# Kernel optimization log

Hardware: AMD Instinct MI355X
Metric: run time of the kernel (lower is better)

The kernel has to match this reference:

```python
import jax, jax.numpy as jnp
import numpy as np

POS_W, NEG_W = 2.0, 40.0
MARGIN, THRESH = 0.1, 0.5


def setup_inputs() -> dict:
    key = jax.random.key(0)
    k1, k2 = jax.random.split(key)
    B, D, C = 4096, 128, 100
    batch = jax.random.normal(k1, (B, D), dtype=jnp.float32)
    # metric-learning embeddings are L2-normalized -> sim in [-1, 1]
    batch = batch / jnp.linalg.norm(batch, axis=1, keepdims=True)
    labels = jax.random.randint(k2, (B,), 0, C)
    return {"batch": batch, "labels": labels}


def reference(batch, labels):
    B = batch.shape[0]
    sim = batch @ batch.T  # [B, B]
    eq = labels[:, None] == labels[None, :]
    not_self = ~jnp.eye(B, dtype=bool)
    pos_mask = eq & not_self   # positives, excluding anchor itself
    neg_mask = ~eq             # negatives

    # per-row hardest thresholds (masked min/max)
    min_pos = jnp.min(jnp.where(pos_mask, sim, jnp.inf), axis=1)   # [B]
    max_neg = jnp.max(jnp.where(neg_mask, sim, -jnp.inf), axis=1)  # [B]

    neg_keep = neg_mask & (sim + MARGIN > min_pos[:, None])
    pos_keep = pos_mask & (sim - MARGIN < max_neg[:, None])

    # masked exponentials: exp(-inf) = 0 keeps it overflow-safe
    pos_sum = jnp.sum(jnp.exp(jnp.where(pos_keep, -POS_W * (sim - THRESH), -jnp.inf)), axis=1)
    neg_sum = jnp.sum(jnp.exp(jnp.where(neg_keep, NEG_W * (sim - THRESH), -jnp.inf)), axis=1)

    row_loss = jnp.log1p(pos_sum) / POS_W + jnp.log1p(neg_sum) / NEG_W  # [B]

    # original skips rows where either kept-set is empty
    valid = jnp.any(pos_keep, axis=1) & jnp.any(neg_keep, axis=1)
    n_valid = jnp.maximum(jnp.sum(valid), 1)
    return jnp.sum(jnp.where(valid, row_loss, 0.0)) / n_valid
```

## Files before the change

kernel.cpp:

```cpp
#include <hip/hip_runtime.h>
#include <math.h>

#define Bsz 4096
#define Dk 128
#define RPB 32
#define CS 16
#define CPB (Bsz / CS)
#define THREADS 256
#define WAVES 4
#define CPW (CPB / WAVES)
#define CT (CPW / 16)
#define RT (RPB / 16)

typedef __attribute__((ext_vector_type(8))) short short8;
typedef __attribute__((ext_vector_type(4))) float f32x4;

__device__ __forceinline__ unsigned short f2bf(float f) {
  unsigned u = __float_as_uint(f);
  u = (u + 0x7fffu + ((u >> 16) & 1u)) >> 16;
  return (unsigned short)u;
}

__global__ __launch_bounds__(256)
void convert_kernel(const float* __restrict__ X, short* __restrict__ Xt) {
  int i = blockIdx.x * 256 + threadIdx.x;
  int col = i >> 4, kb = i & 15;
  const float4* q = (const float4*)(X + col * Dk + kb * 8);
  float4 v0 = q[0], v1 = q[1];
  short8 r;
  r[0] = (short)f2bf(v0.x); r[1] = (short)f2bf(v0.y);
  r[2] = (short)f2bf(v0.z); r[3] = (short)f2bf(v0.w);
  r[4] = (short)f2bf(v1.x); r[5] = (short)f2bf(v1.y);
  r[6] = (short)f2bf(v1.z); r[7] = (short)f2bf(v1.w);
  *(short8*)(Xt + (size_t)(kb * Bsz + col) * 8) = r;
}

__device__ __forceinline__ short8 ldfrag(const short* __restrict__ Xt, int col, int ks, int lg) {
  return *(const short8*)(Xt + (size_t)(((ks << 2) + lg) * Bsz + col) * 8);
}

template<int PHASE>
__global__ __launch_bounds__(THREADS, 4)
void sweep(const short* __restrict__ Xt, const int* __restrict__ labels,
           const float* __restrict__ min_part, const float* __restrict__ max_part,
           float* __restrict__ out0, float* __restrict__ out1,
           float* __restrict__ vld) {
  const int tid = threadIdx.x;
  const int w  = tid >> 6;
  const int l  = tid & 63;
  const int lg = l >> 4;
  const int lr = l & 15;
  const int by = blockIdx.x / CS;
  const int bx = blockIdx.x % CS;
  const int r0 = by * RPB;
  const int c0 = bx * CPB + w * CPW;

  __shared__ float red[2][WAVES][RPB];
  __shared__ float thp_s[RPB], thn_s[RPB];

  if (PHASE == 1) {
    if (tid < RPB) {
      int r = r0 + tid;
      float mnr = INFINITY, mxr = -INFINITY;
#pragma unroll
      for (int b = 0; b < CS; ++b) {
        mnr = fminf(mnr, min_part[b * Bsz + r]);
        mxr = fmaxf(mxr, max_part[b * Bsz + r]);
      }
      thp_s[tid] = mxr + 0.1f;
      thn_s[tid] = mnr - 0.1f;
      if (bx == 0) vld[r] = (mnr - 0.1f < mxr) ? 1.0f : 0.0f;
    }
  }

  short8 afrag[RT][4];
  for (int rt = 0; rt < RT; ++rt)
    for (int ks = 0; ks < 4; ++ks)
      afrag[rt][ks] = ldfrag(Xt, r0 + rt * 16 + lr, ks, lg);

  int labr[RT * 4];
  for (int rt = 0; rt < RT; ++rt)
    for (int rg = 0; rg < 4; ++rg)
      labr[rt * 4 + rg] = labels[r0 + rt * 16 + lg * 4 + rg];

  float tp[RT * 4], tn[RT * 4];
  if (PHASE == 1) {
    __syncthreads();
    for (int rt = 0; rt < RT; ++rt)
      for (int rg = 0; rg < 4; ++rg) {
        int rl = rt * 16 + lg * 4 + rg;
        tp[rt * 4 + rg] = thp_s[rl];
        tn[rt * 4 + rg] = thn_s[rl];
      }
  }

  float a0[RT * 4], a1[RT * 4];
  for (int i = 0; i < RT * 4; ++i) {
    a0[i] = (PHASE == 0) ? INFINITY  : 0.f;
    a1[i] = (PHASE == 0) ? -INFINITY : 0.f;
  }

#pragma unroll
  for (int ct = 0; ct < CT; ++ct) {
    const int ctc  = c0 + ct * 16;
    const int colv = ctc + lr;
    short8 bfrag[4];
    for (int ks = 0; ks < 4; ++ks) bfrag[ks] = ldfrag(Xt, colv, ks, lg);
    const int labc = labels[colv];

    for (int rt = 0; rt < RT; ++rt) {
      f32x4 acc = {0.f, 0.f, 0.f, 0.f};
      for (int ks = 0; ks < 4; ++ks)
        acc = __builtin_amdgcn_mfma_f32_16x16x32_bf16(afrag[rt][ks], bfrag[ks], acc, 0, 0, 0);
      const bool diag = (ctc == r0 + rt * 16);
      for (int rg = 0; rg < 4; ++rg) {
        int   i    = rt * 4 + rg;
        float s    = acc[rg];
        bool  eq   = (labc == labr[i]);
        bool  self = diag && (lr == lg * 4 + rg);
        if (PHASE == 0) {
          if (eq && !self) a0[i] = fminf(a0[i], s);
          if (!eq)         a1[i] = fmaxf(a1[i], s);
        } else {
          bool  kp   = eq && !self && (s < tp[i]);
          bool  kn   = (!eq) && (s > tn[i]);
          float argp = fmaf(s, -2.885390082f, 1.442695041f);
          float argn = fmaf(s, 57.70780163f, -28.85390082f);
          float e = exp2f(kp ? argp : argn);
          a0[i] += kp ? e : 0.f;
          a1[i] += kn ? e : 0.f;
        }
      }
    }
  }

  for (int i = 0; i < RT * 4; ++i) {
    for (int m = 1; m < 16; m <<= 1) {
      float o0 = __shfl_xor(a0[i], m, 64);
      float o1 = __shfl_xor(a1[i], m, 64);
      if (PHASE == 0) { a0[i] = fminf(a0[i], o0); a1[i] = fmaxf(a1[i], o1); }
      else            { a0[i] += o0;              a1[i] += o1; }
    }
  }
  if (lr == 0)
    for (int i = 0; i < RT * 4; ++i) {
      int rt = i >> 2, rg = i & 3;
      red[0][w][rt * 16 + lg * 4 + rg] = a0[i];
      red[1][w][rt * 16 + lg * 4 + rg] = a1[i];
    }
  __syncthreads();

  if (tid < RPB) {
    if (PHASE == 0) {
      float v0 = INFINITY, v1 = -INFINITY;
      for (int ww = 0; ww < WAVES; ++ww) {
        v0 = fminf(v0, red[0][ww][tid]);
        v1 = fmaxf(v1, red[1][ww][tid]);
      }
      out0[bx * Bsz + r0 + tid] = v0;
      out1[bx * Bsz + r0 + tid] = v1;
    } else {
      float v0 = 0.f, v1 = 0.f;
      for (int ww = 0; ww < WAVES; ++ww) {
        v0 += red[0][ww][tid];
        v1 += red[1][ww][tid];
      }
      out0[bx * Bsz + r0 + tid] = v0;
      out1[bx * Bsz + r0 + tid] = v1;
    }
  }
}

__global__ __launch_bounds__(1024)
void finalize(const float* __restrict__ pos_part, const float* __restrict__ neg_part,
              const float* __restrict__ vld, float* __restrict__ out) {
  int tid = threadIdx.x;
  float s = 0.f, c = 0.f;
  for (int r = tid; r < Bsz; r += 1024) {
    float ps = 0.f, ns = 0.f;
#pragma unroll
    for (int b = 0; b < CS; ++b) {
      ps += pos_part[b * Bsz + r];
      ns += neg_part[b * Bsz + r];
    }
    if (vld[r] > 0.f) {
      s += log1pf(ps) * 0.5f + log1pf(ns) * 0.025f;
      c += 1.f;
    }
  }
  for (int m = 1; m < 64; m <<= 1) {
    s += __shfl_xor(s, m, 64);
    c += __shfl_xor(c, m, 64);
  }
  __shared__ float rs[16], rc[16];
  int w = tid >> 6, lz = tid & 63;
  if (lz == 0) { rs[w] = s; rc[w] = c; }
  __syncthreads();
  if (tid == 0) {
    float ts = 0.f, tc = 0.f;
    for (int i = 0; i < 16; ++i) { ts += rs[i]; tc += rc[i]; }
    out[0] = ts / fmaxf(tc, 1.0f);
  }
}

extern "C" void kernel_launch(void* const* d_in, const int* in_sizes, int n_in,
                              void* d_out, int out_size, void* d_ws, size_t ws_size,
                              hipStream_t stream) {
  const float* X      = (const float*)d_in[0];
  const int*   labels = (const int*)d_in[1];

  char* ws = (char*)d_ws;
  short* Xt       = (short*)ws;
  float* min_part = (float*)(ws + 1048576);
  float* max_part = (float*)(ws + 1048576 + 262144);
  float* pos_part = (float*)(ws + 1048576 + 524288);
  float* neg_part = (float*)(ws + 1048576 + 786432);
  float* vld      = (float*)(ws + 2097152);

  convert_kernel<<<256, 256, 0, stream>>>(X, Xt);
  sweep<0><<<(Bsz / RPB) * CS, THREADS, 0, stream>>>(Xt, labels, nullptr, nullptr,
                                                     min_part, max_part, nullptr);
  sweep<1><<<(Bsz / RPB) * CS, THREADS, 0, stream>>>(Xt, labels, min_part, max_part,
                                                     pos_part, neg_part, vld);
  finalize<<<1, 1024, 0, stream>>>(pos_part, neg_part, vld, (float*)d_out);
}
```

Before: 47.29 us.

## Fuse both similarity sweeps into one kernel with full-row blocks

Replaces the two separate sweep kernels, which exchanged per-row partial min/max across column-split blocks through global memory, with one kernel. Each 1024-thread block owns 16 full rows, so thresholds are reduced in shared memory and the second pass follows a block barrier. The row loss is computed in-kernel, which also simplifies finalize. This removes a launch and the global partial round trips, but each wave now computes a single 16-row tile per MFMA group, halving A-fragment reuse. Launch bounds of 1024 threads with 4 blocks per CU may also limit registers, and the column loops are no longer explicitly unrolled.

```diff
diff --git a/kernel.cpp b/kernel.cpp
--- a/kernel.cpp
+++ b/kernel.cpp
@@ -3,14 +3,12 @@
 
 #define Bsz 4096
 #define Dk 128
-#define RPB 32
-#define CS 16
-#define CPB (Bsz / CS)
-#define THREADS 256
-#define WAVES 4
-#define CPW (CPB / WAVES)
+#define RPB 16
+#define NBLK (Bsz / RPB)
+#define THREADS 1024
+#define NW 16
+#define CPW (Bsz / NW)
 #define CT (CPW / 16)
-#define RT (RPB / 16)
 
 typedef __attribute__((ext_vector_type(8))) short short8;
 typedef __attribute__((ext_vector_type(4))) float f32x4;
@@ -39,154 +37,133 @@
   return *(const short8*)(Xt + (size_t)(((ks << 2) + lg) * Bsz + col) * 8);
 }
 
-template<int PHASE>
 __global__ __launch_bounds__(THREADS, 4)
-void sweep(const short* __restrict__ Xt, const int* __restrict__ labels,
-           const float* __restrict__ min_part, const float* __restrict__ max_part,
-           float* __restrict__ out0, float* __restrict__ out1,
-           float* __restrict__ vld) {
+void mono(const short* __restrict__ Xt, const int* __restrict__ labels,
+          float* __restrict__ row_loss, float* __restrict__ row_valid) {
   const int tid = threadIdx.x;
   const int w  = tid >> 6;
   const int l  = tid & 63;
   const int lg = l >> 4;
   const int lr = l & 15;
-  const int by = blockIdx.x / CS;
-  const int bx = blockIdx.x % CS;
-  const int r0 = by * RPB;
-  const int c0 = bx * CPB + w * CPW;
+  const int r0 = blockIdx.x * RPB;
 
-  __shared__ float red[2][WAVES][RPB];
-  __shared__ float thp_s[RPB], thn_s[RPB];
+  __shared__ float red[2][NW][RPB];
+  __shared__ float thp_s[RPB], thn_s[RPB], vld_s[RPB];
 
-  if (PHASE == 1) {
-    if (tid < RPB) {
-      int r = r0 + tid;
-      float mnr = INFINITY, mxr = -INFINITY;
-#pragma unroll
-      for (int b = 0; b < CS; ++b) {
-        mnr = fminf(mnr, min_part[b * Bsz + r]);
-        mxr = fmaxf(mxr, max_part[b * Bsz + r]);
-      }
-      thp_s[tid] = mxr + 0.1f;
-      thn_s[tid] = mnr - 0.1f;
-      if (bx == 0) vld[r] = (mnr - 0.1f < mxr) ? 1.0f : 0.0f;
-    }
-  }
+  short8 afrag[4];
+  for (int ks = 0; ks < 4; ++ks) afrag[ks] = ldfrag(Xt, r0 + lr, ks, lg);
+  int labr[4];
+  for (int rg = 0; rg < 4; ++rg) labr[rg] = labels[r0 + lg * 4 + rg];
 
-  short8 afrag[RT][4];
-  for (int rt = 0; rt < RT; ++rt)
-    for (int ks = 0; ks < 4; ++ks)
-      afrag[rt][ks] = ldfrag(Xt, r0 + rt * 16 + lr, ks, lg);
+  float mnp[4], mxn[4];
+  for (int rg = 0; rg < 4; ++rg) { mnp[rg] = INFINITY; mxn[rg] = -INFINITY; }
 
-  int labr[RT * 4];
-  for (int rt = 0; rt < RT; ++rt)
-    for (int rg = 0; rg < 4; ++rg)
-      labr[rt * 4 + rg] = labels[r0 + rt * 16 + lg * 4 + rg];
-
-  float tp[RT * 4], tn[RT * 4];
-  if (PHASE == 1) {
-    __syncthreads();
-    for (int rt = 0; rt < RT; ++rt)
-      for (int rg = 0; rg < 4; ++rg) {
-        int rl = rt * 16 + lg * 4 + rg;
-        tp[rt * 4 + rg] = thp_s[rl];
-        tn[rt * 4 + rg] = thn_s[rl];
-      }
-  }
-
-  float a0[RT * 4], a1[RT * 4];
-  for (int i = 0; i < RT * 4; ++i) {
-    a0[i] = (PHASE == 0) ? INFINITY  : 0.f;
-    a1[i] = (PHASE == 0) ? -INFINITY : 0.f;
-  }
-
-#pragma unroll
   for (int ct = 0; ct < CT; ++ct) {
-    const int ctc  = c0 + ct * 16;
+    const int ctc  = w * CPW + ct * 16;
     const int colv = ctc + lr;
     short8 bfrag[4];
     for (int ks = 0; ks < 4; ++ks) bfrag[ks] = ldfrag(Xt, colv, ks, lg);
     const int labc = labels[colv];
 
-    for (int rt = 0; rt < RT; ++rt) {
-      f32x4 acc = {0.f, 0.f, 0.f, 0.f};
-      for (int ks = 0; ks < 4; ++ks)
-        acc = __builtin_amdgcn_mfma_f32_16x16x32_bf16(afrag[rt][ks], bfrag[ks], acc, 0, 0, 0);
-      const bool diag = (ctc == r0 + rt * 16);
-      for (int rg = 0; rg < 4; ++rg) {
-        int   i    = rt * 4 + rg;
-        float s    = acc[rg];
-        bool  eq   = (labc == labr[i]);
-        bool  self = diag && (lr == lg * 4 + rg);
-        if (PHASE == 0) {
-          if (eq && !self) a0[i] = fminf(a0[i], s);
-          if (!eq)         a1[i] = fmaxf(a1[i], s);
-        } else {
-          bool  kp   = eq && !self && (s < tp[i]);
-          bool  kn   = (!eq) && (s > tn[i]);
-          float argp = fmaf(s, -2.885390082f, 1.442695041f);
-          float argn = fmaf(s, 57.70780163f, -28.85390082f);
-          float e = exp2f(kp ? argp : argn);
-          a0[i] += kp ? e : 0.f;
-          a1[i] += kn ? e : 0.f;
-        }
-      }
+    f32x4 acc = {0.f, 0.f, 0.f, 0.f};
+    for (int ks = 0; ks < 4; ++ks)
+      acc = __builtin_amdgcn_mfma_f32_16x16x32_bf16(afrag[ks], bfrag[ks], acc, 0, 0, 0);
+    const bool diag = (ctc == r0);
+    for (int rg = 0; rg < 4; ++rg) {
+      float s    = acc[rg];
+      bool  eq   = (labc == labr[rg]);
+      bool  self = diag && (lr == lg * 4 + rg);
+      if (eq && !self) mnp[rg] = fminf(mnp[rg], s);
+      if (!eq)         mxn[rg] = fmaxf(mxn[rg], s);
     }
   }
-
-  for (int i = 0; i < RT * 4; ++i) {
+  for (int rg = 0; rg < 4; ++rg) {
     for (int m = 1; m < 16; m <<= 1) {
-      float o0 = __shfl_xor(a0[i], m, 64);
-      float o1 = __shfl_xor(a1[i], m, 64);
-      if (PHASE == 0) { a0[i] = fminf(a0[i], o0); a1[i] = fmaxf(a1[i], o1); }
-      else            { a0[i] += o0;              a1[i] += o1; }
+      mnp[rg] = fminf(mnp[rg], __shfl_xor(mnp[rg], m, 64));
+      mxn[rg] = fmaxf(mxn[rg], __shfl_xor(mxn[rg], m, 64));
     }
   }
   if (lr == 0)
-    for (int i = 0; i < RT * 4; ++i) {
-      int rt = i >> 2, rg = i & 3;
-      red[0][w][rt * 16 + lg * 4 + rg] = a0[i];
-      red[1][w][rt * 16 + lg * 4 + rg] = a1[i];
+    for (int rg = 0; rg < 4; ++rg) {
+      red[0][w][lg * 4 + rg] = mnp[rg];
+      red[1][w][lg * 4 + rg] = mxn[rg];
     }
   __syncthreads();
 
   if (tid < RPB) {
-    if (PHASE == 0) {
-      float v0 = INFINITY, v1 = -INFINITY;
-      for (int ww = 0; ww < WAVES; ++ww) {
-        v0 = fminf(v0, red[0][ww][tid]);
-        v1 = fmaxf(v1, red[1][ww][tid]);
-      }
-      out0[bx * Bsz + r0 + tid] = v0;
-      out1[bx * Bsz + r0 + tid] = v1;
-    } else {
-      float v0 = 0.f, v1 = 0.f;
-      for (int ww = 0; ww < WAVES; ++ww) {
-        v0 += red[0][ww][tid];
-        v1 += red[1][ww][tid];
-      }
-      out0[bx * Bsz + r0 + tid] = v0;
-      out1[bx * Bsz + r0 + tid] = v1;
+    float a = INFINITY, b = -INFINITY;
+    for (int ww = 0; ww < NW; ++ww) {
+      a = fminf(a, red[0][ww][tid]);
+      b = fmaxf(b, red[1][ww][tid]);
     }
+    thp_s[tid] = b + 0.1f;
+    thn_s[tid] = a - 0.1f;
+    vld_s[tid] = (a - 0.1f < b) ? 1.f : 0.f;
+  }
+  __syncthreads();
+
+  float tp[4], tn[4];
+  for (int rg = 0; rg < 4; ++rg) {
+    tp[rg] = thp_s[lg * 4 + rg];
+    tn[rg] = thn_s[lg * 4 + rg];
+  }
+  float ap[4] = {0.f, 0.f, 0.f, 0.f}, an[4] = {0.f, 0.f, 0.f, 0.f};
+
+  for (int ct = 0; ct < CT; ++ct) {
+    const int ctc  = w * CPW + ct * 16;
+    const int colv = ctc + lr;
+    short8 bfrag[4];
+    for (int ks = 0; ks < 4; ++ks) bfrag[ks] = ldfrag(Xt, colv, ks, lg);
+    const int labc = labels[colv];
+
+    f32x4 acc = {0.f, 0.f, 0.f, 0.f};
+    for (int ks = 0; ks < 4; ++ks)
+      acc = __builtin_amdgcn_mfma_f32_16x16x32_bf16(afrag[ks], bfrag[ks], acc, 0, 0, 0);
+    const bool diag = (ctc == r0);
+    for (int rg = 0; rg < 4; ++rg) {
+      float s    = acc[rg];
+      bool  eq   = (labc == labr[rg]);
+      bool  self = diag && (lr == lg * 4 + rg);
+      bool  kp   = eq && !self && (s < tp[rg]);
+      bool  kn   = (!eq) && (s > tn[rg]);
+      float argp = fmaf(s, -2.885390082f, 1.442695041f);
+      float argn = fmaf(s, 57.70780163f, -28.85390082f);
+      float e = exp2f(kp ? argp : argn);
+      ap[rg] += kp ? e : 0.f;
+      an[rg] += kn ? e : 0.f;
+    }
+  }
+  for (int rg = 0; rg < 4; ++rg) {
+    for (int m = 1; m < 16; m <<= 1) {
+      ap[rg] += __shfl_xor(ap[rg], m, 64);
+      an[rg] += __shfl_xor(an[rg], m, 64);
+    }
+  }
+  __syncthreads();
+  if (lr == 0)
+    for (int rg = 0; rg < 4; ++rg) {
+      red[0][w][lg * 4 + rg] = ap[rg];
+      red[1][w][lg * 4 + rg] = an[rg];
+    }
+  __syncthreads();
+
+  if (tid < RPB) {
+    float P = 0.f, N = 0.f;
+    for (int ww = 0; ww < NW; ++ww) { P += red[0][ww][tid]; N += red[1][ww][tid]; }
+    bool v = vld_s[tid] > 0.f;
+    row_loss[r0 + tid]  = v ? (log1pf(P) * 0.5f + log1pf(N) * 0.025f) : 0.f;
+    row_valid[r0 + tid] = v ? 1.f : 0.f;
   }
 }
 
 __global__ __launch_bounds__(1024)
-void finalize(const float* __restrict__ pos_part, const float* __restrict__ neg_part,
-              const float* __restrict__ vld, float* __restrict__ out) {
+void finalize(const float* __restrict__ row_loss, const float* __restrict__ row_valid,
+              float* __restrict__ out) {
   int tid = threadIdx.x;
   float s = 0.f, c = 0.f;
   for (int r = tid; r < Bsz; r += 1024) {
-    float ps = 0.f, ns = 0.f;
-#pragma unroll
-    for (int b = 0; b < CS; ++b) {
-      ps += pos_part[b * Bsz + r];
-      ns += neg_part[b * Bsz + r];
-    }
-    if (vld[r] > 0.f) {
-      s += log1pf(ps) * 0.5f + log1pf(ns) * 0.025f;
-      c += 1.f;
-    }
+    s += row_loss[r];
+    c += row_valid[r];
   }
   for (int m = 1; m < 64; m <<= 1) {
     s += __shfl_xor(s, m, 64);
@@ -210,17 +187,11 @@
   const int*   labels = (const int*)d_in[1];
 
   char* ws = (char*)d_ws;
-  short* Xt       = (short*)ws;
-  float* min_part = (float*)(ws + 1048576);
-  float* max_part = (float*)(ws + 1048576 + 262144);
-  float* pos_part = (float*)(ws + 1048576 + 524288);
-  float* neg_part = (float*)(ws + 1048576 + 786432);
-  float* vld      = (float*)(ws + 2097152);
+  short* Xt        = (short*)ws;
+  float* row_loss  = (float*)(ws + 1048576);
+  float* row_valid = (float*)(ws + 1048576 + 16384);
 
   convert_kernel<<<256, 256, 0, stream>>>(X, Xt);
-  sweep<0><<<(Bsz / RPB) * CS, THREADS, 0, stream>>>(Xt, labels, nullptr, nullptr,
-                                                     min_part, max_part, nullptr);
-  sweep<1><<<(Bsz / RPB) * CS, THREADS, 0, stream>>>(Xt, labels, min_part, max_part,
-                                                     pos_part, neg_part, vld);
-  finalize<<<1, 1024, 0, stream>>>(pos_part, neg_part, vld, (float*)d_out);
+  mono<<<NBLK, THREADS, 0, stream>>>(Xt, labels, row_loss, row_valid);
+  finalize<<<1, 1024, 0, stream>>>(row_loss, row_valid, (float*)d_out);
 }
```

Result: faster. 38.58 us (median of 2 runs) (-18.4%).
